# Kernel tuning notes

Hardware: AMD Instinct MI355X
Metric: run time of the kernel (lower is better)

## Reference

```python
import jax, jax.numpy as jnp
import numpy as np

N, T, D, H = 4, 2048, 1024, 16
DK = D // H

def setup_inputs() -> dict:
    key = jax.random.key(0)
    k1, k2, k3 = jax.random.split(key, 3)
    z = jax.random.normal(k1, (N, T, D), dtype=jnp.float32)
    Wqkv = jax.random.normal(k2, (D, 3 * D), dtype=jnp.float32) * 0.01
    Wout = jax.random.normal(k3, (D, D), dtype=jnp.float32) * 0.01
    return {"z": z, "Wqkv": Wqkv, "Wout": Wout}

def reference(z, Wqkv, Wout):
    n, t, d = z.shape
    scale = DK ** -0.5
    qkv = z @ Wqkv  # [N,T,3D]
    q, k, v = jnp.split(qkv, 3, axis=-1)
    # [N,T,D] -> [N,H,T,dk]
    q = q.reshape(n, t, H, DK).transpose(0, 2, 1, 3)
    k = k.reshape(n, t, H, DK).transpose(0, 2, 1, 3)
    v = v.reshape(n, t, H, DK).transpose(0, 2, 1, 3)
    attn = jnp.einsum('nhqd,nhkd->nhqk', q, k) * scale
    causal = jnp.tril(jnp.ones((t, t), dtype=bool))
    attn = jnp.where(causal, attn, -jnp.inf)
    attn = jax.nn.softmax(attn, axis=-1)
    out = jnp.einsum('nhqk,nhkd->nhqd', attn, v)  # [N,H,T,dk]
    out = out.transpose(0, 2, 1, 3).reshape(n, t, d)
    return out @ Wout
```

## Files before the change

kernel.cpp:

```cpp
#include <hip/hip_runtime.h>
#include <hip/hip_bf16.h>

typedef __bf16 bf16;
typedef __bf16 bf16x8 __attribute__((ext_vector_type(8)));
typedef float f32x4 __attribute__((ext_vector_type(4)));

#define N_B 4
#define T_S 2048
#define D_M 1024
#define H_N 16
#define D_K 64
#define D3 3072
#define NEG_BIG (-1e30f)
#define QSCALE 0.18033688011112042f

#if __has_builtin(__builtin_amdgcn_exp2f)
#define EXP2(x) __builtin_amdgcn_exp2f(x)
#else
#define EXP2(x) exp2f(x)
#endif

__device__ __forceinline__ void gload_lds16(const bf16* g, bf16* l) {
    __builtin_amdgcn_global_load_lds((const __attribute__((address_space(1))) void*)g,
                                     (__attribute__((address_space(3))) void*)l, 16, 0, 0);
}

__device__ __forceinline__ bool probe_fp32(const void* p) {
    const unsigned int* w = (const unsigned int*)p;
    int weird = 0;
#pragma unroll
    for (int i = 0; i < 16; ++i) {
        unsigned int v = w[i];
        unsigned int e = (v >> 7) & 0xFFu;
        if ((v & 0xFFFFu) != 0u && (e < 100u || e > 140u)) weird++;
    }
    return weird >= 4;
}

__global__ __launch_bounds__(256) void prep(const void* __restrict__ z, bf16* __restrict__ zb,
                                            const void* __restrict__ Wqkv, bf16* __restrict__ WqkvT,
                                            const void* __restrict__ Wout, bf16* __restrict__ WoutT) {
    __shared__ bf16 tile[32][33];
    const int b = blockIdx.x;
    const int t = threadIdx.x;

    if (b < 4096) {
        const int i = (b * 256 + t) * 8;
        if (probe_fp32(z)) {
            const float* zf = (const float*)z;
            float4 u0 = *(const float4*)(zf + i);
            float4 u1 = *(const float4*)(zf + i + 4);
            union { uint4 q; bf16 h[8]; } pk;
            pk.h[0] = (bf16)u0.x; pk.h[1] = (bf16)u0.y;
            pk.h[2] = (bf16)u0.z; pk.h[3] = (bf16)u0.w;
            pk.h[4] = (bf16)u1.x; pk.h[5] = (bf16)u1.y;
            pk.h[6] = (bf16)u1.z; pk.h[7] = (bf16)u1.w;
            *(uint4*)(zb + i) = pk.q;
        } else {
            *(uint4*)(zb + i) = ((const uint4*)z)[b * 256 + t];
        }
        return;
    }

    const void* in; bf16* out; int R, C, c0, r0;
    if (b < 7168) {
        int idx = b - 4096;
        in = Wqkv; out = WqkvT; R = 1024; C = 3072;
        c0 = (idx % 96) * 32; r0 = (idx / 96) * 32;
    } else {
        int idx = b - 7168;
        in = Wout; out = WoutT; R = 1024; C = 1024;
        c0 = (idx & 31) * 32; r0 = (idx >> 5) * 32;
    }
    const int tx = t & 31, ty = t >> 5;
    if (probe_fp32(in)) {
        const float* inf_ = (const float*)in;
        for (int i = 0; i < 4; ++i)
            tile[ty + i * 8][tx] = (bf16)inf_[(size_t)(r0 + ty + i * 8) * C + c0 + tx];
    } else {
        const bf16* inb = (const bf16*)in;
        for (int i = 0; i < 4; ++i)
            tile[ty + i * 8][tx] = inb[(size_t)(r0 + ty + i * 8) * C + c0 + tx];
    }
    __syncthreads();
    for (int i = 0; i < 4; ++i)
        out[(size_t)(c0 + ty + i * 8) * R + r0 + tx] = tile[tx][ty + i * 8];
}

__global__ __launch_bounds__(512, 2) void gemm256(const bf16* __restrict__ A,
                                                  const bf16* __restrict__ Bt,
                                                  void* __restrict__ C,
                                                  bf16* __restrict__ Kf,
                                                  bf16* __restrict__ Vf,
                                                  int M, int N, int K,
                                                  int modeC) {
    __shared__ bf16 As[3][256 * 64];
    __shared__ bf16 Bs[3][128 * 64];
    const int t = threadIdx.x;
    const int m0 = blockIdx.y * 256, n0 = blockIdx.x * 128;
    const int w = t >> 6, lane = t & 63, quad = lane >> 4, l15 = lane & 15;
    const int wr = (w >> 1) * 64, wc = (w & 1) * 64;
    const int sr = t >> 3;
    const int sg = ((t & 7) ^ (sr & 7)) * 8;
    const int xorL = (l15 & 7) * 8;

    const bf16* a0 = A + (size_t)(m0 + sr) * K + sg;
    const bf16* a1 = A + (size_t)(m0 + 64 + sr) * K + sg;
    const bf16* a2 = A + (size_t)(m0 + 128 + sr) * K + sg;
    const bf16* a3 = A + (size_t)(m0 + 192 + sr) * K + sg;
    const bf16* b0 = Bt + (size_t)(n0 + sr) * K + sg;
    const bf16* b1 = Bt + (size_t)(n0 + 64 + sr) * K + sg;
    const int ldsOff = w * 512;

    f32x4 acc[4][4];
    const f32x4 zero4 = {0.f, 0.f, 0.f, 0.f};
#pragma unroll
    for (int i = 0; i < 4; ++i)
#pragma unroll
        for (int j = 0; j < 4; ++j) acc[i][j] = zero4;

    const int nt = K >> 6;

    gload_lds16(a0, &As[0][0 * 4096 + ldsOff]);
    gload_lds16(a1, &As[0][1 * 4096 + ldsOff]);
    gload_lds16(a2, &As[0][2 * 4096 + ldsOff]);
    gload_lds16(a3, &As[0][3 * 4096 + ldsOff]);
    gload_lds16(b0, &Bs[0][0 * 4096 + ldsOff]);
    gload_lds16(b1, &Bs[0][1 * 4096 + ldsOff]);
    gload_lds16(a0 + 64, &As[1][0 * 4096 + ldsOff]);
    gload_lds16(a1 + 64, &As[1][1 * 4096 + ldsOff]);
    gload_lds16(a2 + 64, &As[1][2 * 4096 + ldsOff]);
    gload_lds16(a3 + 64, &As[1][3 * 4096 + ldsOff]);
    gload_lds16(b0 + 64, &Bs[1][0 * 4096 + ldsOff]);
    gload_lds16(b1 + 64, &Bs[1][1 * 4096 + ldsOff]);

    int cur = 0;
    for (int tt = 0; tt < nt; ++tt) {
        asm volatile("s_waitcnt lgkmcnt(0)" ::: "memory");
        if (tt + 1 < nt) {
            asm volatile("s_waitcnt vmcnt(6)" ::: "memory");
        } else {
            asm volatile("s_waitcnt vmcnt(0)" ::: "memory");
        }
        __builtin_amdgcn_sched_barrier(0);
        __builtin_amdgcn_s_barrier();
        __builtin_amdgcn_sched_barrier(0);

        if (tt + 2 < nt) {
            int pf = cur + 2; if (pf >= 3) pf -= 3;
            const int kpf = (tt + 2) << 6;
            gload_lds16(a0 + kpf, &As[pf][0 * 4096 + ldsOff]);
            gload_lds16(a1 + kpf, &As[pf][1 * 4096 + ldsOff]);
            gload_lds16(a2 + kpf, &As[pf][2 * 4096 + ldsOff]);
            gload_lds16(a3 + kpf, &As[pf][3 * 4096 + ldsOff]);
            gload_lds16(b0 + kpf, &Bs[pf][0 * 4096 + ldsOff]);
            gload_lds16(b1 + kpf, &Bs[pf][1 * 4096 + ldsOff]);
        }

        const bf16* Ac = As[cur];
        const bf16* Bc = Bs[cur];
#pragma unroll
        for (int kk = 0; kk < 2; ++kk) {
            const int colOff = (kk * 32 + quad * 8) ^ xorL;
            bf16x8 af[4], bfv[4];
#pragma unroll
            for (int i = 0; i < 4; ++i)
                af[i] = *(const bf16x8*)(Ac + (wr + i * 16 + l15) * 64 + colOff);
#pragma unroll
            for (int j = 0; j < 4; ++j)
                bfv[j] = *(const bf16x8*)(Bc + (wc + j * 16 + l15) * 64 + colOff);
            __builtin_amdgcn_s_setprio(1);
#pragma unroll
            for (int i = 0; i < 4; ++i)
#pragma unroll
                for (int j = 0; j < 4; ++j)
                    acc[i][j] = __builtin_amdgcn_mfma_f32_16x16x32_bf16(af[i], bfv[j], acc[i][j], 0, 0, 0);
            __builtin_amdgcn_s_setprio(0);
        }
        cur = cur + 1; if (cur == 3) cur = 0;
    }

    if (modeC == 1) {
        float* Cf = (float*)C;
        for (int i = 0; i < 4; ++i)
            for (int fc = 0; fc < 4; ++fc)
                for (int r = 0; r < 4; ++r)
                    Cf[(size_t)(m0 + wr + i * 16 + quad * 4 + r) * N
                       + (n0 + wc + fc * 16 + l15)] = acc[i][fc][r];
    } else if (n0 < 1024) {
        bf16* q = (bf16*)C;
        for (int i = 0; i < 4; ++i)
            for (int fc = 0; fc < 4; ++fc)
                for (int r = 0; r < 4; ++r)
                    q[(size_t)(m0 + wr + i * 16 + quad * 4 + r) * 1024
                      + (n0 + wc + fc * 16 + l15)] = (bf16)(acc[i][fc][r] * QSCALE);
    } else if (n0 < 2048) {
        for (int i = 0; i < 4; ++i) {
            int rowb = m0 + wr + i * 16 + quad * 4;
            int nb = rowb >> 11, tt = rowb & 2047;
            int kt = tt >> 6, f = (tt >> 4) & 3, l15k = tt & 15;
            for (int fc = 0; fc < 4; ++fc) {
                int col = n0 + wc + fc * 16 + l15 - 1024;
                int h = col >> 6, dk = col & 63;
                int ks = dk >> 5, qdk = (dk >> 3) & 3, j = dk & 7;
                size_t base = ((size_t)((nb * 16 + h) * 32 + kt) * 8 + ks * 4 + f) * 512 + j;
                for (int r = 0; r < 4; ++r)
                    Kf[base + (qdk * 16 + l15k + r) * 8] = (bf16)acc[i][fc][r];
            }
        }
    } else {
        for (int i = 0; i < 4; ++i) {
            int rowb = m0 + wr + i * 16 + quad * 4;
            int nb = rowb >> 11, tt = rowb & 2047;
            int kt = tt >> 6, ks = (tt >> 5) & 1, qdv = (tt >> 3) & 3, j0 = tt & 7;
            for (int fc = 0; fc < 4; ++fc) {
                int col = n0 + wc + fc * 16 + l15 - 2048;
                int h = col >> 6, dl = col & 63;
                int fv = dl >> 4, l15v = dl & 15;
                union { ushort4 u; bf16 hh[4]; } pk;
                for (int r = 0; r < 4; ++r) pk.hh[r] = (bf16)acc[i][fc][r];
                *(ushort4*)(Vf + ((size_t)((nb * 16 + h) * 32 + kt) * 8 + ks * 4 + fv) * 512
                            + (qdv * 16 + l15v) * 8 + j0) = pk.u;
            }
        }
    }
}

#define LDP 72
__global__ __launch_bounds__(256, 2) void attn_fused(const bf16* __restrict__ q,
                                                     const bf16* __restrict__ Kf,
                                                     const bf16* __restrict__ Vf,
                                                     bf16* __restrict__ attn_out) {
    __shared__ bf16 Pl[4 * 32 * LDP];

    const int b = blockIdx.x;
    const int head = b & 63;
    const int qp = b >> 6;
    const int n = head >> 4, h = head & 15;
    const int t = threadIdx.x;
    const int w = t >> 6, lane = t & 63, qd = lane >> 4, l15 = lane & 15;
    const int r = (w + qp + head) & 3;
    const int qt = (r < 2) ? qp : (31 - qp);
    const int q0w = qt * 64 + (r & 1) * 32;
    const size_t rowBase = (size_t)n * T_S;
    const bf16* KfH = Kf + (size_t)head * 32 * 4096;
    const bf16* VfH = Vf + (size_t)head * 32 * 4096;
    bf16* Plw = Pl + w * 32 * LDP;

    bf16x8 bQ[2][2];
#pragma unroll
    for (int qh = 0; qh < 2; ++qh)
#pragma unroll
        for (int ks = 0; ks < 2; ++ks)
            bQ[qh][ks] = *(const bf16x8*)(q + (rowBase + q0w + qh * 16 + l15) * 1024
                                          + h * 64 + ks * 32 + qd * 8);

    float l_lane[2] = {0.f, 0.f};
    f32x4 oacc[2][4];
    const f32x4 zero4 = {0.f, 0.f, 0.f, 0.f};
#pragma unroll
    for (int qh = 0; qh < 2; ++qh)
#pragma unroll
        for (int fd = 0; fd < 4; ++fd) oacc[qh][fd] = zero4;

    const int ktmax = (q0w + 31) >> 6;

    bf16x8 aK[2][4];
#pragma unroll
    for (int fr = 0; fr < 8; ++fr)
        aK[fr >> 2][fr & 3] = *(const bf16x8*)(KfH + fr * 512 + lane * 8);

    for (int kt = 0; kt <= ktmax; ++kt) {
        const int k0r = kt * 64;
        const bf16* VfT = VfH + (size_t)kt * 4096;

        bf16x8 aV[2][4];
#pragma unroll
        for (int fr = 0; fr < 8; ++fr)
            aV[fr >> 2][fr & 3] = *(const bf16x8*)(VfT + fr * 512 + lane * 8);

        f32x4 sacc[2][4];
#pragma unroll
        for (int qh = 0; qh < 2; ++qh)
#pragma unroll
            for (int fc = 0; fc < 4; ++fc) sacc[qh][fc] = zero4;
#pragma unroll
        for (int ks = 0; ks < 2; ++ks)
#pragma unroll
            for (int fc = 0; fc < 4; ++fc) {
                sacc[0][fc] = __builtin_amdgcn_mfma_f32_16x16x32_bf16(aK[ks][fc], bQ[0][ks], sacc[0][fc], 0, 0, 0);
                sacc[1][fc] = __builtin_amdgcn_mfma_f32_16x16x32_bf16(aK[ks][fc], bQ[1][ks], sacc[1][fc], 0, 0, 0);
            }

        if (kt < ktmax) {
            const bf16* KfN = KfH + (size_t)(kt + 1) * 4096;
#pragma unroll
            for (int fr = 0; fr < 8; ++fr)
                aK[fr >> 2][fr & 3] = *(const bf16x8*)(KfN + fr * 512 + lane * 8);
        }

        if (k0r + 63 > q0w) {
#pragma unroll
            for (int qh = 0; qh < 2; ++qh) {
                const int qq = q0w + qh * 16 + l15;
#pragma unroll
                for (int fc = 0; fc < 4; ++fc)
#pragma unroll
                    for (int rr = 0; rr < 4; ++rr)
                        if (k0r + fc * 16 + qd * 4 + rr > qq) sacc[qh][fc][rr] = NEG_BIG;
            }
        }

#pragma unroll
        for (int qh = 0; qh < 2; ++qh) {
            float rs = 0.f;
#pragma unroll
            for (int fc = 0; fc < 4; ++fc) {
                union { ushort4 u; bf16 hh[4]; } pk;
#pragma unroll
                for (int rr = 0; rr < 4; ++rr) {
                    float p = EXP2(sacc[qh][fc][rr]);
                    rs += p;
                    pk.hh[rr] = (bf16)p;
                }
                *(ushort4*)(Plw + (qh * 16 + l15) * LDP + fc * 16 + qd * 4) = pk.u;
            }
            l_lane[qh] += rs;
        }

#pragma unroll
        for (int ks = 0; ks < 2; ++ks) {
            bf16x8 bP0 = *(const bf16x8*)(Plw + l15 * LDP + ks * 32 + qd * 8);
            bf16x8 bP1 = *(const bf16x8*)(Plw + (16 + l15) * LDP + ks * 32 + qd * 8);
#pragma unroll
            for (int fd = 0; fd < 4; ++fd) {
                oacc[0][fd] = __builtin_amdgcn_mfma_f32_16x16x32_bf16(aV[ks][fd], bP0, oacc[0][fd], 0, 0, 0);
                oacc[1][fd] = __builtin_amdgcn_mfma_f32_16x16x32_bf16(aV[ks][fd], bP1, oacc[1][fd], 0, 0, 0);
            }
        }
    }

#pragma unroll
    for (int qh = 0; qh < 2; ++qh) {
        float l = l_lane[qh];
        l += __shfl_xor(l, 16, 64);
        l += __shfl_xor(l, 32, 64);
        float inv = 1.f / l;
#pragma unroll
        for (int fd = 0; fd < 4; ++fd) {
            union { ushort4 u; bf16 hh[4]; } pk;
#pragma unroll
            for (int rr = 0; rr < 4; ++rr) pk.hh[rr] = (bf16)(oacc[qh][fd][rr] * inv);
            *(ushort4*)(attn_out + (rowBase + q0w + qh * 16 + l15) * D_M
                        + h * D_K + fd * 16 + qd * 4) = pk.u;
        }
    }
}

extern "C" void kernel_launch(void* const* d_in, const int* in_sizes, int n_in,
                              void* d_out, int out_size, void* d_ws, size_t ws_size,
                              hipStream_t stream) {
    const void* z    = d_in[0];
    const void* Wqkv = d_in[1];
    const void* Wout = d_in[2];

    char* ws = (char*)d_ws;
    bf16* q     = (bf16*)(ws + 256);
    bf16* attn  = (bf16*)(ws + 256 + 16777216);
    bf16* zb    = attn;
    bf16* WqkvT = (bf16*)(ws + 256 + 2 * 16777216);
    bf16* WoutT = (bf16*)(ws + 256 + 2 * 16777216 + 6291456);

    bf16* Kf = (bf16*)d_out;
    bf16* Vf = Kf + 8388608;

    prep<<<dim3(8192), 256, 0, stream>>>(z, zb, Wqkv, WqkvT, Wout, WoutT);

    gemm256<<<dim3(D3 / 128, (N_B * T_S) / 256), 512, 0, stream>>>(
        zb, WqkvT, q, Kf, Vf, N_B * T_S, D3, D_M, 2);

    attn_fused<<<dim3(64 * 16), 256, 0, stream>>>(q, Kf, Vf, attn);

    gemm256<<<dim3(D_M / 128, (N_B * T_S) / 256), 512, 0, stream>>>(
        attn, WoutT, d_out, Kf, Vf, N_B * T_S, D_M, D_M, 1);
}
```

Measured before the change: 243.5 us.

## Interleave GEMM prefetch loads with LDS reads in ping-pong barrier schedule

The GEMM main loop is restructured into two explicit K-half phases. Each phase issues its LDS fragment reads, then half of the next-tile global-to-LDS prefetch loads, and brackets the MFMA block with workgroup barriers. The wait and barrier for the first tile move before the loop, and the per-iteration vmcnt wait moves into the second phase. The aim is to overlap global loads with LDS reads and MFMA work, in a pattern similar to ping-pong scheduling, at the cost of more barriers per iteration.

```diff
diff --git a/kernel.cpp b/kernel.cpp
--- a/kernel.cpp
+++ b/kernel.cpp
@@ -127,41 +127,31 @@
     gload_lds16(a3, &As[0][3 * 4096 + ldsOff]);
     gload_lds16(b0, &Bs[0][0 * 4096 + ldsOff]);
     gload_lds16(b1, &Bs[0][1 * 4096 + ldsOff]);
-    gload_lds16(a0 + 64, &As[1][0 * 4096 + ldsOff]);
-    gload_lds16(a1 + 64, &As[1][1 * 4096 + ldsOff]);
-    gload_lds16(a2 + 64, &As[1][2 * 4096 + ldsOff]);
-    gload_lds16(a3 + 64, &As[1][3 * 4096 + ldsOff]);
-    gload_lds16(b0 + 64, &Bs[1][0 * 4096 + ldsOff]);
-    gload_lds16(b1 + 64, &Bs[1][1 * 4096 + ldsOff]);
+    if (nt > 1) {
+        gload_lds16(a0 + 64, &As[1][0 * 4096 + ldsOff]);
+        gload_lds16(a1 + 64, &As[1][1 * 4096 + ldsOff]);
+        gload_lds16(a2 + 64, &As[1][2 * 4096 + ldsOff]);
+        gload_lds16(a3 + 64, &As[1][3 * 4096 + ldsOff]);
+        gload_lds16(b0 + 64, &Bs[1][0 * 4096 + ldsOff]);
+        gload_lds16(b1 + 64, &Bs[1][1 * 4096 + ldsOff]);
+        asm volatile("s_waitcnt vmcnt(6)" ::: "memory");
+    } else {
+        asm volatile("s_waitcnt vmcnt(0)" ::: "memory");
+    }
+    __builtin_amdgcn_sched_barrier(0);
+    __builtin_amdgcn_s_barrier();
+    __builtin_amdgcn_sched_barrier(0);
 
     int cur = 0;
     for (int tt = 0; tt < nt; ++tt) {
-        asm volatile("s_waitcnt lgkmcnt(0)" ::: "memory");
-        if (tt + 1 < nt) {
-            asm volatile("s_waitcnt vmcnt(6)" ::: "memory");
-        } else {
-            asm volatile("s_waitcnt vmcnt(0)" ::: "memory");
-        }
-        __builtin_amdgcn_sched_barrier(0);
-        __builtin_amdgcn_s_barrier();
-        __builtin_amdgcn_sched_barrier(0);
-
-        if (tt + 2 < nt) {
-            int pf = cur + 2; if (pf >= 3) pf -= 3;
-            const int kpf = (tt + 2) << 6;
-            gload_lds16(a0 + kpf, &As[pf][0 * 4096 + ldsOff]);
-            gload_lds16(a1 + kpf, &As[pf][1 * 4096 + ldsOff]);
-            gload_lds16(a2 + kpf, &As[pf][2 * 4096 + ldsOff]);
-            gload_lds16(a3 + kpf, &As[pf][3 * 4096 + ldsOff]);
-            gload_lds16(b0 + kpf, &Bs[pf][0 * 4096 + ldsOff]);
-            gload_lds16(b1 + kpf, &Bs[pf][1 * 4096 + ldsOff]);
-        }
-
         const bf16* Ac = As[cur];
         const bf16* Bc = Bs[cur];
-#pragma unroll
-        for (int kk = 0; kk < 2; ++kk) {
-            const int colOff = (kk * 32 + quad * 8) ^ xorL;
+        int pf = cur + 2; if (pf >= 3) pf -= 3;
+        const bool do_pf = (tt + 2 < nt);
+        const int kpf = (tt + 2) << 6;
+
+        {
+            const int colOff = (quad * 8) ^ xorL;
             bf16x8 af[4], bfv[4];
 #pragma unroll
             for (int i = 0; i < 4; ++i)
@@ -169,6 +159,15 @@
 #pragma unroll
             for (int j = 0; j < 4; ++j)
                 bfv[j] = *(const bf16x8*)(Bc + (wc + j * 16 + l15) * 64 + colOff);
+            if (do_pf) {
+                gload_lds16(a0 + kpf, &As[pf][0 * 4096 + ldsOff]);
+                gload_lds16(a1 + kpf, &As[pf][1 * 4096 + ldsOff]);
+                gload_lds16(a2 + kpf, &As[pf][2 * 4096 + ldsOff]);
+            }
+            __builtin_amdgcn_sched_barrier(0);
+            __builtin_amdgcn_s_barrier();
+            asm volatile("s_waitcnt lgkmcnt(0)" ::: "memory");
+            __builtin_amdgcn_sched_barrier(0);
             __builtin_amdgcn_s_setprio(1);
 #pragma unroll
             for (int i = 0; i < 4; ++i)
@@ -176,6 +175,42 @@
                 for (int j = 0; j < 4; ++j)
                     acc[i][j] = __builtin_amdgcn_mfma_f32_16x16x32_bf16(af[i], bfv[j], acc[i][j], 0, 0, 0);
             __builtin_amdgcn_s_setprio(0);
+            __builtin_amdgcn_sched_barrier(0);
+            __builtin_amdgcn_s_barrier();
+            __builtin_amdgcn_sched_barrier(0);
+        }
+
+        {
+            const int colOff = (32 + quad * 8) ^ xorL;
+            bf16x8 af[4], bfv[4];
+#pragma unroll
+            for (int i = 0; i < 4; ++i)
+                af[i] = *(const bf16x8*)(Ac + (wr + i * 16 + l15) * 64 + colOff);
+#pragma unroll
+            for (int j = 0; j < 4; ++j)
+                bfv[j] = *(const bf16x8*)(Bc + (wc + j * 16 + l15) * 64 + colOff);
+            if (do_pf) {
+                gload_lds16(a3 + kpf, &As[pf][3 * 4096 + ldsOff]);
+                gload_lds16(b0 + kpf, &Bs[pf][0 * 4096 + ldsOff]);
+                gload_lds16(b1 + kpf, &Bs[pf][1 * 4096 + ldsOff]);
+                asm volatile("s_waitcnt vmcnt(6)" ::: "memory");
+            } else {
+                asm volatile("s_waitcnt vmcnt(0)" ::: "memory");
+            }
+            __builtin_amdgcn_sched_barrier(0);
+            __builtin_amdgcn_s_barrier();
+            asm volatile("s_waitcnt lgkmcnt(0)" ::: "memory");
+            __builtin_amdgcn_sched_barrier(0);
+            __builtin_amdgcn_s_setprio(1);
+#pragma unroll
+            for (int i = 0; i < 4; ++i)
+#pragma unroll
+                for (int j = 0; j < 4; ++j)
+                    acc[i][j] = __builtin_amdgcn_mfma_f32_16x16x32_bf16(af[i], bfv[j], acc[i][j], 0, 0, 0);
+            __builtin_amdgcn_s_setprio(0);
+            __builtin_amdgcn_sched_barrier(0);
+            __builtin_amdgcn_s_barrier();
+            __builtin_amdgcn_sched_barrier(0);
         }
         cur = cur + 1; if (cur == 3) cur = 0;
     }
```

New measurement: 233.1 us. -4.3%, faster.
